# Optimization experiments

Hardware: AMD Instinct MI355X
Metric: run time of the kernel (lower is better)

The kernel has to match this reference:

```python
import jax, jax.numpy as jnp
import numpy as np

T, D, H, E, K = 8192, 2048, 7168, 8, 2


def setup_inputs() -> dict:
    key = jax.random.key(0)
    ks = jax.random.split(key, 5)
    s = 0.02
    return {
        "x": jax.random.normal(ks[0], (T, D), jnp.float32),
        "gate_w": jax.random.normal(ks[1], (E, D), jnp.float32) * s,
        "w1": jax.random.normal(ks[2], (E, H, D), jnp.float32) * s,
        "w2": jax.random.normal(ks[3], (E, H, D), jnp.float32) * s,
        "w3": jax.random.normal(ks[4], (E, H, D), jnp.float32) * s,
    }


def reference(x, gate_w, w1, w2, w3):
    # gate logits [T, E]
    logits = x @ gate_w.T
    vals, idx = jax.lax.top_k(logits, K)                      # [T, K]
    w = jax.nn.softmax(vals.astype(jnp.float32), axis=-1).astype(x.dtype)
    # per-token routing weight for each expert (0 if not selected) [T, E]
    tok = jnp.arange(x.shape[0])
    expert_w = jnp.zeros((x.shape[0], E), x.dtype).at[tok[:, None], idx].add(w)

    # scan over experts: dense SwiGLU per expert, weighted accumulate
    def body(acc, ws):
        w1e, w2e, w3e, we = ws  # [H,D],[H,D],[H,D],[T]
        y = (jax.nn.silu(x @ w1e.T) * (x @ w3e.T)) @ w2e      # [T, D]
        return acc + we[:, None] * y, None

    res, _ = jax.lax.scan(body, jnp.zeros_like(x), (w1, w2, w3, expert_w.T))
    return res
```

## Files before the change

kernel.cpp:

```cpp
#include <hip/hip_runtime.h>

#define TT   8192
#define DDIM 2048
#define HDIM 7168
#define NEXP 8
#define MT   32
#define NT1  (HDIM / 128)
#define NT2  (DDIM / 256)
#define NTILE_MAX 72

typedef __attribute__((ext_vector_type(8))) short bf16x8;
typedef __attribute__((ext_vector_type(8))) short short8v;
typedef __attribute__((ext_vector_type(4))) short short4v;
typedef __attribute__((ext_vector_type(4))) float f32x4;

__device__ __forceinline__ unsigned short f2bf(float f) {
  unsigned int u = __builtin_bit_cast(unsigned int, f);
  u += 0x7fffu + ((u >> 16) & 1u);
  return (unsigned short)(u >> 16);
}

__device__ __forceinline__ void gload_lds16(const void* gp, void* lp) {
  __builtin_amdgcn_global_load_lds((__attribute__((address_space(1))) void*)gp,
                                   (__attribute__((address_space(3))) void*)lp,
                                   16, 0, 0);
}

__device__ __forceinline__ void mfma16(f32x4& c, bf16x8 a, bf16x8 b) {
  c = __builtin_amdgcn_mfma_f32_16x16x32_bf16(a, b, c, 0, 0, 0);
}

__device__ __forceinline__ void wg_barrier() {
  asm volatile("" ::: "memory");
  __builtin_amdgcn_s_barrier();
  asm volatile("" ::: "memory");
}

#define PH(H, BA, BB, RDB, STG, SRCP, SOFF, VM)                              \
  do {                                                                       \
    if (RDB) {                                                               \
      _Pragma("unroll")                                                      \
      for (int n = 0; n < 4; ++n)                                            \
        bfr[n] = *(const bf16x8*)(smem + (BB) + rB + n * 1024);              \
    }                                                                        \
    _Pragma("unroll")                                                        \
    for (int m = 0; m < 4; ++m)                                              \
      af[m] = *(const bf16x8*)(smem + (BA) + rA + ((H) + m) * 1024);         \
    if ((STG) >= 0) {                                                        \
      gload_lds16(SRCP[0] + (SOFF), smem + (STG) + wid * 2048);              \
      gload_lds16(SRCP[1] + (SOFF), smem + (STG) + wid * 2048 + 1024);       \
    }                                                                        \
    wg_barrier();                                                            \
    __builtin_amdgcn_s_setprio(1);                                           \
    _Pragma("unroll")                                                        \
    for (int n = 0; n < 4; ++n) {                                            \
      _Pragma("unroll")                                                      \
      for (int m = 0; m < 4; ++m)                                            \
        mfma16(acc[(H) + m][n], af[m], bfr[n]);                              \
    }                                                                        \
    __builtin_amdgcn_s_setprio(0);                                           \
    if ((VM) == 6) asm volatile("s_waitcnt vmcnt(6)" ::: "memory");          \
    if ((VM) == 0) asm volatile("s_waitcnt vmcnt(0)" ::: "memory");          \
    wg_barrier();                                                            \
  } while (0)

#define ITER_FULL(kb)                                                        \
  PH(0, 0,     32768,  1, 81920,  asrc, (kb) + 192, -1);                     \
  PH(4, 0,     32768,  0, 32768,  bsrc, (kb) + 256, -1);                     \
  PH(0, 16384, 49152,  1, 0,      asrc, (kb) + 256, -1);                     \
  PH(4, 16384, 49152,  0, 49152,  bsrc, (kb) + 320,  6);                     \
  PH(0, 65536, 98304,  1, 16384,  asrc, (kb) + 320, -1);                     \
  PH(4, 65536, 98304,  0, 98304,  bsrc, (kb) + 384, -1);                     \
  PH(0, 81920, 114688, 1, 65536,  asrc, (kb) + 384, -1);                     \
  PH(4, 81920, 114688, 0, 114688, bsrc, (kb) + 448,  6);

#define ITER_LAST(kb)                                                        \
  PH(0, 0,     32768,  1, 81920,  asrc, (kb) + 192, -1);                     \
  PH(4, 0,     32768,  0, -1,     asrc, 0,          -1);                     \
  PH(0, 16384, 49152,  1, -1,     asrc, 0,          -1);                     \
  PH(4, 16384, 49152,  0, -1,     asrc, 0,           0);                     \
  PH(0, 65536, 98304,  1, -1,     asrc, 0,          -1);                     \
  PH(4, 65536, 98304,  0, -1,     asrc, 0,          -1);                     \
  PH(0, 81920, 114688, 1, -1,     asrc, 0,          -1);                     \
  PH(4, 81920, 114688, 0, -1,     asrc, 0,          -1);

#define PROLOGUE()                                                           \
  do {                                                                       \
    gload_lds16(asrc[0] + 0,   smem + 0      + wid * 2048);                  \
    gload_lds16(asrc[1] + 0,   smem + 0      + wid * 2048 + 1024);           \
    gload_lds16(bsrc[0] + 0,   smem + 32768  + wid * 2048);                  \
    gload_lds16(bsrc[1] + 0,   smem + 32768  + wid * 2048 + 1024);           \
    gload_lds16(asrc[0] + 64,  smem + 16384  + wid * 2048);                  \
    gload_lds16(asrc[1] + 64,  smem + 16384  + wid * 2048 + 1024);           \
    gload_lds16(bsrc[0] + 64,  smem + 49152  + wid * 2048);                  \
    gload_lds16(bsrc[1] + 64,  smem + 49152  + wid * 2048 + 1024);           \
    gload_lds16(bsrc[0] + 128, smem + 98304  + wid * 2048);                  \
    gload_lds16(bsrc[1] + 128, smem + 98304  + wid * 2048 + 1024);           \
    gload_lds16(asrc[0] + 128, smem + 65536  + wid * 2048);                  \
    gload_lds16(asrc[1] + 128, smem + 65536  + wid * 2048 + 1024);           \
    gload_lds16(bsrc[0] + 192, smem + 114688 + wid * 2048);                  \
    gload_lds16(bsrc[1] + 192, smem + 114688 + wid * 2048 + 1024);           \
    asm volatile("s_waitcnt vmcnt(6)" ::: "memory");                         \
    wg_barrier();                                                            \
  } while (0)

__global__ __launch_bounds__(256) void cvt_bf16_kernel(const float* __restrict__ src,
                                                       unsigned short* __restrict__ dst,
                                                       long n8) {
  long i = (long)blockIdx.x * 256 + threadIdx.x;
  long stride = (long)gridDim.x * 256;
  for (; i < n8; i += stride) {
    float4 a = ((const float4*)src)[i * 2];
    float4 b = ((const float4*)src)[i * 2 + 1];
    short8v s;
    s[0] = (short)f2bf(a.x); s[1] = (short)f2bf(a.y);
    s[2] = (short)f2bf(a.z); s[3] = (short)f2bf(a.w);
    s[4] = (short)f2bf(b.x); s[5] = (short)f2bf(b.y);
    s[6] = (short)f2bf(b.z); s[7] = (short)f2bf(b.w);
    ((short8v*)dst)[i] = s;
  }
}

__global__ __launch_bounds__(256) void gate_kernel(const float* __restrict__ x,
                                                   const float* __restrict__ gw,
                                                   int* __restrict__ route_e,
                                                   float* __restrict__ route_w,
                                                   int* __restrict__ counts) {
  int t = blockIdx.x;
  int tid = threadIdx.x;
  const float* xr = x + (size_t)t * DDIM;
  float p[NEXP];
#pragma unroll
  for (int e = 0; e < NEXP; ++e) p[e] = 0.f;
#pragma unroll
  for (int c = 0; c < DDIM / (256 * 4); ++c) {
    int d = (c * 256 + tid) * 4;
    float4 xv = *(const float4*)(xr + d);
#pragma unroll
    for (int e = 0; e < NEXP; ++e) {
      float4 wv = *(const float4*)(gw + (size_t)e * DDIM + d);
      p[e] += xv.x * wv.x + xv.y * wv.y + xv.z * wv.z + xv.w * wv.w;
    }
  }
  __shared__ float red[NEXP][4];
  int lane = tid & 63, wid = tid >> 6;
#pragma unroll
  for (int e = 0; e < NEXP; ++e) {
    float v = p[e];
    for (int o = 32; o > 0; o >>= 1) v += __shfl_down(v, o);
    if (lane == 0) red[e][wid] = v;
  }
  __syncthreads();
  if (tid == 0) {
    float lg[NEXP];
#pragma unroll
    for (int e = 0; e < NEXP; ++e) lg[e] = red[e][0] + red[e][1] + red[e][2] + red[e][3];
    int i0 = 0;
#pragma unroll
    for (int e = 1; e < NEXP; ++e) if (lg[e] > lg[i0]) i0 = e;
    int i1 = -1;
#pragma unroll
    for (int e = 0; e < NEXP; ++e) {
      if (e == i0) continue;
      if (i1 < 0 || lg[e] > lg[i1]) i1 = e;
    }
    float w0 = 1.f / (1.f + __expf(lg[i1] - lg[i0]));
    float w1 = 1.f - w0;
    route_e[t * 2 + 0] = i0;  route_e[t * 2 + 1] = i1;
    route_w[t * 2 + 0] = w0;  route_w[t * 2 + 1] = w1;
    atomicAdd(&counts[i0], 1);
    atomicAdd(&counts[i1], 1);
  }
}

__global__ void scan_kernel(const int* __restrict__ counts, int* __restrict__ offsets,
                            int* __restrict__ cursor, int* __restrict__ tmap) {
  if (threadIdx.x == 0 && blockIdx.x == 0) {
    int o = 0, idx = 0;
    for (int e = 0; e < NEXP; ++e) {
      offsets[e] = o; cursor[e] = o;
      int c = counts[e]; o += c;
      for (int t = 0; t * 256 < c && idx < NTILE_MAX; ++t) tmap[1 + idx++] = (e << 16) | t;
    }
    tmap[0] = idx;
  }
}

__global__ __launch_bounds__(256) void scatter_kernel(const int* __restrict__ route_e,
                                                      const float* __restrict__ route_w,
                                                      int* __restrict__ cursor,
                                                      int* __restrict__ tok_list,
                                                      float* __restrict__ tok_w) {
  int t = blockIdx.x * 256 + threadIdx.x;
  if (t >= TT) return;
#pragma unroll
  for (int s = 0; s < 2; ++s) {
    int e = route_e[t * 2 + s];
    int p = atomicAdd(&cursor[e], 1);
    tok_list[p] = t;
    tok_w[p] = route_w[t * 2 + s];
  }
}

__global__ __launch_bounds__(256) void transpose_w2_kernel(const float* __restrict__ w2,
                                                           unsigned short* __restrict__ w2t,
                                                           int expert_fixed) {
  int e = expert_fixed >= 0 ? expert_fixed : (int)blockIdx.z;
  const float* src = w2 + (size_t)e * HDIM * DDIM;
  unsigned short* dst = w2t + (expert_fixed >= 0 ? (size_t)0 : (size_t)e * DDIM * HDIM);
  int h0 = blockIdx.x * 64, d0 = blockIdx.y * 64;
  __shared__ __align__(8) unsigned short tile[64 * 66];
  int tid = threadIdx.x;
  int hr = tid >> 2;
#pragma unroll
  for (int j = 0; j < 4; ++j) {
    int f4 = (tid & 3) + j * 4;
    float4 v = *(const float4*)(src + (size_t)(h0 + hr) * DDIM + d0 + f4 * 4);
    unsigned int lo = (unsigned int)f2bf(v.x) | ((unsigned int)f2bf(v.y) << 16);
    unsigned int hi = (unsigned int)f2bf(v.z) | ((unsigned int)f2bf(v.w) << 16);
    char* bp = (char*)tile + hr * 132 + f4 * 8;
    *(unsigned int*)bp = lo;
    *(unsigned int*)(bp + 4) = hi;
  }
  __syncthreads();
  int dr = tid >> 2;
  int hbase = (tid & 3) * 16;
  unsigned short vals[16];
#pragma unroll
  for (int i = 0; i < 16; ++i)
    vals[i] = *(unsigned short*)((char*)tile + (hbase + i) * 132 + dr * 2);
  unsigned short* op = dst + (size_t)(d0 + dr) * HDIM + h0 + hbase;
  short8v s0, s1;
#pragma unroll
  for (int i = 0; i < 8; ++i) { s0[i] = (short)vals[i]; s1[i] = (short)vals[i + 8]; }
  *(short8v*)(op) = s0;
  *(short8v*)(op + 8) = s1;
}

__global__ __launch_bounds__(512, 2) void gemm1_kernel(
    const unsigned short* __restrict__ xbf, const unsigned short* __restrict__ w1b,
    const unsigned short* __restrict__ w3b, const int* __restrict__ tok_list,
    const int* __restrict__ counts, const int* __restrict__ offsets,
    const int* __restrict__ tmap,
    unsigned short* __restrict__ g, int expert_fixed) {
  __shared__ __align__(16) char smem[133120];
  constexpr int NI = DDIM / 128;

  int nwg = gridDim.x;
  int orig = blockIdx.x;
  int wg = (orig & 7) * (nwg >> 3) + (orig >> 3);
  int e, mbase, nt;
  if (expert_fixed >= 0) {
    e = expert_fixed;
    mbase = (wg & (MT - 1)) * 256;
    nt = (wg >> 5) % NT1;
  } else {
    int tl = wg % NTILE_MAX;
    nt = wg / NTILE_MAX;
    if (tl >= tmap[0]) return;
    int pk = tmap[1 + tl];
    e = pk >> 16;
    mbase = (pk & 0xffff) * 256;
  }
  int cnt = counts[e];
  if (mbase >= cnt) return;
  int off = offsets[e];
  int gshift = expert_fixed >= 0 ? 0 : off;
  int rows = cnt - mbase; if (rows > 256) rows = 256;

  const unsigned short* w1e = expert_fixed >= 0 ? w1b : w1b + (size_t)e * HDIM * DDIM;
  const unsigned short* w3e = expert_fixed >= 0 ? w3b : w3b + (size_t)e * HDIM * DDIM;

  int tid = threadIdx.x, lane = tid & 63, wid = tid >> 6;
  int wr = wid >> 2, wc = wid & 3;

  int r16 = lane >> 2;
  int csrc = (lane & 3) ^ ((lane >> 3) & 3);
  const char* asrc[2]; const char* bsrc[2];
#pragma unroll
  for (int j = 0; j < 2; ++j) {
    int r = wid * 32 + j * 16 + r16;
    int m = mbase + r; if (m > cnt - 1) m = cnt - 1;
    int tok = tok_list[off + m];
    asrc[j] = (const char*)xbf + (size_t)tok * (DDIM * 2) + csrc * 16;
    const char* base = (r < 128)
        ? (const char*)w1e + (size_t)(nt * 128 + r) * (DDIM * 2)
        : (const char*)w3e + (size_t)(nt * 128 + r - 128) * (DDIM * 2);
    bsrc[j] = base + csrc * 16;
  }
  int rA = (wr * 128 + (lane & 15)) * 64 + (((lane >> 4) ^ ((lane >> 1) & 3)) * 16);
  int rB = (wc * 64  + (lane & 15)) * 64 + (((lane >> 4) ^ ((lane >> 1) & 3)) * 16);

  f32x4 zv = {0.f, 0.f, 0.f, 0.f};
  f32x4 acc[8][4];
#pragma unroll
  for (int m = 0; m < 8; ++m)
#pragma unroll
    for (int n = 0; n < 4; ++n) acc[m][n] = zv;
  bf16x8 af[4], bfr[4];

  PROLOGUE();
#pragma unroll 1
  for (int i = 0; i < NI - 1; ++i) {
    size_t kb = (size_t)i * 256;
    ITER_FULL(kb);
  }
  {
    size_t kb = (size_t)(NI - 1) * 256;
    ITER_LAST(kb);
  }

  float* hb = (float*)smem;
  if (wc < 2) {
#pragma unroll
    for (int m = 0; m < 8; ++m)
#pragma unroll
      for (int q = 0; q < 4; ++q) {
        int row = wr * 128 + m * 16 + (lane >> 4) * 4 + q;
        int col = wc * 64 + (lane & 15);
#pragma unroll
        for (int n = 0; n < 4; ++n)
          hb[row * 130 + col + n * 16] = acc[m][n][q];
      }
  }
  asm volatile("s_waitcnt lgkmcnt(0)" ::: "memory");
  wg_barrier();
  if (wc >= 2) {
#pragma unroll
    for (int m = 0; m < 8; ++m)
#pragma unroll
      for (int q = 0; q < 4; ++q) {
        int row = wr * 128 + m * 16 + (lane >> 4) * 4 + q;
        if (row >= rows) continue;
        size_t grow = (size_t)(mbase + row + gshift);
        int colbase = (wc - 2) * 64 + (lane & 15);
        unsigned short* gp = g + grow * HDIM + nt * 128 + colbase;
#pragma unroll
        for (int n = 0; n < 4; ++n) {
          float h1 = hb[row * 130 + colbase + n * 16];
          float h3 = acc[m][n][q];
          float gv = (h1 / (1.f + __expf(-h1))) * h3;
          gp[n * 16] = f2bf(gv);
        }
      }
  }
}

__global__ __launch_bounds__(512, 2) void gemm2_kernel(
    const unsigned short* __restrict__ g, const unsigned short* __restrict__ w2t,
    const int* __restrict__ tok_list, const float* __restrict__ tok_w,
    const int* __restrict__ counts, const int* __restrict__ offsets,
    const int* __restrict__ tmap,
    float* __restrict__ out, int expert_fixed) {
  __shared__ __align__(16) char smem[131072];
  constexpr int NI = HDIM / 128;

  int nwg = gridDim.x;
  int orig = blockIdx.x;
  int wg = (orig & 7) * (nwg >> 3) + (orig >> 3);
  int e, mbase, nt;
  if (expert_fixed >= 0) {
    e = expert_fixed;
    mbase = (wg & (MT - 1)) * 256;
    nt = (wg >> 5) % NT2;
  } else {
    int tl = wg % NTILE_MAX;
    nt = wg / NTILE_MAX;
    if (tl >= tmap[0]) return;
    int pk = tmap[1 + tl];
    e = pk >> 16;
    mbase = (pk & 0xffff) * 256;
  }
  int cnt = counts[e];
  if (mbase >= cnt) return;
  int off = offsets[e];
  int gshift = expert_fixed >= 0 ? 0 : off;
  int nbase = nt * 256;
  int rows = cnt - mbase; if (rows > 256) rows = 256;
  const unsigned short* w2te = w2t + (expert_fixed >= 0 ? (size_t)0 : (size_t)e * DDIM * HDIM);

  int tid = threadIdx.x, lane = tid & 63, wid = tid >> 6;
  int wr = wid >> 2, wc = wid & 3;

  int r16 = lane >> 2;
  int csrc = (lane & 3) ^ ((lane >> 3) & 3);
  const char* asrc[2]; const char* bsrc[2];
#pragma unroll
  for (int j = 0; j < 2; ++j) {
    int r = wid * 32 + j * 16 + r16;
    int m = mbase + r; if (m > cnt - 1) m = cnt - 1;
    asrc[j] = (const char*)g + (size_t)(m + gshift) * (HDIM * 2) + csrc * 16;
    bsrc[j] = (const char*)w2te + (size_t)(nbase + r) * (HDIM * 2) + csrc * 16;
  }
  int rA = (wr * 128 + (lane & 15)) * 64 + (((lane >> 4) ^ ((lane >> 1) & 3)) * 16);
  int rB = (wc * 64  + (lane & 15)) * 64 + (((lane >> 4) ^ ((lane >> 1) & 3)) * 16);

  f32x4 zv = {0.f, 0.f, 0.f, 0.f};
  f32x4 acc[8][4];
#pragma unroll
  for (int m = 0; m < 8; ++m)
#pragma unroll
    for (int n = 0; n < 4; ++n) acc[m][n] = zv;
  bf16x8 af[4], bfr[4];

  PROLOGUE();
#pragma unroll 1
  for (int i = 0; i < NI - 1; ++i) {
    size_t kb = (size_t)i * 256;
    ITER_FULL(kb);
  }
  {
    size_t kb = (size_t)(NI - 1) * 256;
    ITER_LAST(kb);
  }

#pragma unroll
  for (int m = 0; m < 8; ++m)
#pragma unroll
    for (int q = 0; q < 4; ++q) {
      int row = wr * 128 + m * 16 + (lane >> 4) * 4 + q;
      if (row >= rows) continue;
      int mi = mbase + row;
      int tok = tok_list[off + mi];
      float wt = tok_w[off + mi];
      float* op = out + (size_t)tok * DDIM + nbase + wc * 64 + (lane & 15);
#pragma unroll
      for (int n = 0; n < 4; ++n)
        atomicAdd(op + n * 16, acc[m][n][q] * wt);
    }
}

extern "C" void kernel_launch(void* const* d_in, const int* in_sizes, int n_in,
                              void* d_out, int out_size, void* d_ws, size_t ws_size,
                              hipStream_t stream) {
  const float* x      = (const float*)d_in[0];
  const float* gate_w = (const float*)d_in[1];
  const float* w1     = (const float*)d_in[2];
  const float* w2     = (const float*)d_in[3];
  const float* w3     = (const float*)d_in[4];
  float* out = (float*)d_out;
  char* ws = (char*)d_ws;

  size_t o = 0;
  int* counts  = (int*)(ws + o);
  int* offsets = counts + 8;
  int* cursor  = counts + 16;
  int* tmap    = counts + 24;
  o += 1024;
  int*   route_e = (int*)(ws + o);   o += (size_t)TT * 2 * 4;
  float* route_w = (float*)(ws + o); o += (size_t)TT * 2 * 4;
  int*   tok_list = (int*)(ws + o);  o += (size_t)TT * 2 * 4;
  float* tok_w = (float*)(ws + o);   o += (size_t)TT * 2 * 4;
  unsigned short* xbf = (unsigned short*)(ws + o); o += (size_t)TT * DDIM * 2;
  size_t fixed = o;

  const size_t WSZ = (size_t)HDIM * DDIM;
  const size_t wbf_full = (size_t)NEXP * WSZ * 2;
  const size_t gfull = (size_t)TT * 2 * HDIM * 2;

  hipMemsetAsync(counts, 0, 8 * sizeof(int), stream);
  hipMemsetAsync(out, 0, (size_t)TT * DDIM * sizeof(float), stream);
  cvt_bf16_kernel<<<4096, 256, 0, stream>>>(x, xbf, (long)TT * DDIM / 8);
  gate_kernel<<<TT, 256, 0, stream>>>(x, gate_w, route_e, route_w, counts);
  scan_kernel<<<1, 64, 0, stream>>>(counts, offsets, cursor, tmap);
  scatter_kernel<<<(TT + 255) / 256, 256, 0, stream>>>(route_e, route_w, cursor, tok_list, tok_w);

  if (ws_size >= fixed + 3 * wbf_full + gfull) {
    unsigned short* w1b = (unsigned short*)(ws + fixed);
    unsigned short* w3b = w1b + NEXP * WSZ;
    unsigned short* w2t = w3b + NEXP * WSZ;
    unsigned short* gbuf = w2t + NEXP * WSZ;
    cvt_bf16_kernel<<<8192, 256, 0, stream>>>(w1, w1b, (long)(NEXP * WSZ / 8));
    cvt_bf16_kernel<<<8192, 256, 0, stream>>>(w3, w3b, (long)(NEXP * WSZ / 8));
    transpose_w2_kernel<<<dim3(HDIM / 64, DDIM / 64, NEXP), 256, 0, stream>>>(w2, w2t, -1);
    gemm1_kernel<<<NTILE_MAX * NT1, 512, 0, stream>>>(
        xbf, w1b, w3b, tok_list, counts, offsets, tmap, gbuf, -1);
    gemm2_kernel<<<NTILE_MAX * NT2, 512, 0, stream>>>(
        gbuf, w2t, tok_list, tok_w, counts, offsets, tmap, out, -1);
  } else {
    unsigned short* w1b = (unsigned short*)(ws + fixed);
    unsigned short* w3b = w1b + WSZ;
    unsigned short* w2t = w3b + WSZ;
    unsigned short* gbuf = w2t + WSZ;
    for (int e = 0; e < NEXP; ++e) {
      cvt_bf16_kernel<<<4096, 256, 0, stream>>>(w1 + (size_t)e * WSZ, w1b, (long)(WSZ / 8));
      cvt_bf16_kernel<<<4096, 256, 0, stream>>>(w3 + (size_t)e * WSZ, w3b, (long)(WSZ / 8));
      transpose_w2_kernel<<<dim3(HDIM / 64, DDIM / 64, 1), 256, 0, stream>>>(w2, w2t, e);
      gemm1_kernel<<<MT * NT1, 512, 0, stream>>>(
          xbf, w1b, w3b, tok_list, counts, offsets, tmap, gbuf, e);
      gemm2_kernel<<<MT * NT2, 512, 0, stream>>>(
          gbuf, w2t, tok_list, tok_w, counts, offsets, tmap, out, e);
    }
  }
}
```

Baseline: 2.297 ms.

## Replace gemm2 atomic scatter-add with bf16 slot buffer plus per-token reduce

The second GEMM now writes each routed row's output as bf16 into a per-slot buffer (reusing the w1 bf16 region) instead of doing fp32 atomicAdds into the output. A new reduce kernel combines each token's two slots using the routing weights, which also removes the full output memset on the main path. The gemm2 tile index mapping is also reordered so consecutive workgroups share the same row tile across N tiles. The cost is an extra kernel and bf16 rounding of the per-expert outputs before they are combined.

```diff
diff --git a/kernel.cpp b/kernel.cpp
--- a/kernel.cpp
+++ b/kernel.cpp
@@ -18,6 +18,11 @@
   unsigned int u = __builtin_bit_cast(unsigned int, f);
   u += 0x7fffu + ((u >> 16) & 1u);
   return (unsigned short)(u >> 16);
+}
+
+__device__ __forceinline__ float bf2f(unsigned short h) {
+  unsigned int u = ((unsigned int)h) << 16;
+  return __builtin_bit_cast(float, u);
 }
 
 __device__ __forceinline__ void gload_lds16(const void* gp, void* lp) {
@@ -190,7 +195,8 @@
                                                       const float* __restrict__ route_w,
                                                       int* __restrict__ cursor,
                                                       int* __restrict__ tok_list,
-                                                      float* __restrict__ tok_w) {
+                                                      float* __restrict__ tok_w,
+                                                      int* __restrict__ slot_of) {
   int t = blockIdx.x * 256 + threadIdx.x;
   if (t >= TT) return;
 #pragma unroll
@@ -199,6 +205,7 @@
     int p = atomicAdd(&cursor[e], 1);
     tok_list[p] = t;
     tok_w[p] = route_w[t * 2 + s];
+    slot_of[t * 2 + s] = p;
   }
 }
 
@@ -235,6 +242,30 @@
   for (int i = 0; i < 8; ++i) { s0[i] = (short)vals[i]; s1[i] = (short)vals[i + 8]; }
   *(short8v*)(op) = s0;
   *(short8v*)(op + 8) = s1;
+}
+
+__global__ __launch_bounds__(256) void reduce_kernel(const unsigned short* __restrict__ ybuf,
+                                                     const int* __restrict__ slot_of,
+                                                     const float* __restrict__ route_w,
+                                                     float* __restrict__ out) {
+  int t = blockIdx.x;
+  int d = threadIdx.x * 8;
+  int s0 = slot_of[t * 2 + 0], s1 = slot_of[t * 2 + 1];
+  float w0 = route_w[t * 2 + 0], w1 = route_w[t * 2 + 1];
+  bf16x8 y0 = *(const bf16x8*)(ybuf + (size_t)s0 * DDIM + d);
+  bf16x8 y1 = *(const bf16x8*)(ybuf + (size_t)s1 * DDIM + d);
+  float4 o0, o1;
+  o0.x = w0 * bf2f((unsigned short)y0[0]) + w1 * bf2f((unsigned short)y1[0]);
+  o0.y = w0 * bf2f((unsigned short)y0[1]) + w1 * bf2f((unsigned short)y1[1]);
+  o0.z = w0 * bf2f((unsigned short)y0[2]) + w1 * bf2f((unsigned short)y1[2]);
+  o0.w = w0 * bf2f((unsigned short)y0[3]) + w1 * bf2f((unsigned short)y1[3]);
+  o1.x = w0 * bf2f((unsigned short)y0[4]) + w1 * bf2f((unsigned short)y1[4]);
+  o1.y = w0 * bf2f((unsigned short)y0[5]) + w1 * bf2f((unsigned short)y1[5]);
+  o1.z = w0 * bf2f((unsigned short)y0[6]) + w1 * bf2f((unsigned short)y1[6]);
+  o1.w = w0 * bf2f((unsigned short)y0[7]) + w1 * bf2f((unsigned short)y1[7]);
+  float* op = out + (size_t)t * DDIM + d;
+  *(float4*)op = o0;
+  *(float4*)(op + 4) = o1;
 }
 
 __global__ __launch_bounds__(512, 2) void gemm1_kernel(
@@ -351,7 +382,7 @@
     const int* __restrict__ tok_list, const float* __restrict__ tok_w,
     const int* __restrict__ counts, const int* __restrict__ offsets,
     const int* __restrict__ tmap,
-    float* __restrict__ out, int expert_fixed) {
+    unsigned short* __restrict__ ybuf, float* __restrict__ out, int expert_fixed) {
   __shared__ __align__(16) char smem[131072];
   constexpr int NI = HDIM / 128;
 
@@ -361,11 +392,11 @@
   int e, mbase, nt;
   if (expert_fixed >= 0) {
     e = expert_fixed;
-    mbase = (wg & (MT - 1)) * 256;
-    nt = (wg >> 5) % NT2;
+    nt = wg % NT2;
+    mbase = (wg / NT2) * 256;
   } else {
-    int tl = wg % NTILE_MAX;
-    nt = wg / NTILE_MAX;
+    int tl = wg / NT2;
+    nt = wg % NT2;
     if (tl >= tmap[0]) return;
     int pk = tmap[1 + tl];
     e = pk >> 16;
@@ -414,20 +445,35 @@
     ITER_LAST(kb);
   }
 
-#pragma unroll
-  for (int m = 0; m < 8; ++m)
-#pragma unroll
-    for (int q = 0; q < 4; ++q) {
-      int row = wr * 128 + m * 16 + (lane >> 4) * 4 + q;
-      if (row >= rows) continue;
-      int mi = mbase + row;
-      int tok = tok_list[off + mi];
-      float wt = tok_w[off + mi];
-      float* op = out + (size_t)tok * DDIM + nbase + wc * 64 + (lane & 15);
-#pragma unroll
-      for (int n = 0; n < 4; ++n)
-        atomicAdd(op + n * 16, acc[m][n][q] * wt);
-    }
+  if (ybuf) {
+#pragma unroll
+    for (int m = 0; m < 8; ++m)
+#pragma unroll
+      for (int q = 0; q < 4; ++q) {
+        int row = wr * 128 + m * 16 + (lane >> 4) * 4 + q;
+        if (row >= rows) continue;
+        size_t slot = (size_t)(off + mbase + row);
+        unsigned short* yp = ybuf + slot * DDIM + nbase + wc * 64 + (lane & 15);
+#pragma unroll
+        for (int n = 0; n < 4; ++n)
+          yp[n * 16] = f2bf(acc[m][n][q]);
+      }
+  } else {
+#pragma unroll
+    for (int m = 0; m < 8; ++m)
+#pragma unroll
+      for (int q = 0; q < 4; ++q) {
+        int row = wr * 128 + m * 16 + (lane >> 4) * 4 + q;
+        if (row >= rows) continue;
+        int mi = mbase + row;
+        int tok = tok_list[off + mi];
+        float wt = tok_w[off + mi];
+        float* op = out + (size_t)tok * DDIM + nbase + wc * 64 + (lane & 15);
+#pragma unroll
+        for (int n = 0; n < 4; ++n)
+          atomicAdd(op + n * 16, acc[m][n][q] * wt);
+      }
+  }
 }
 
 extern "C" void kernel_launch(void* const* d_in, const int* in_sizes, int n_in,
@@ -451,6 +497,7 @@
   float* route_w = (float*)(ws + o); o += (size_t)TT * 2 * 4;
   int*   tok_list = (int*)(ws + o);  o += (size_t)TT * 2 * 4;
   float* tok_w = (float*)(ws + o);   o += (size_t)TT * 2 * 4;
+  int*   slot_of = (int*)(ws + o);   o += (size_t)TT * 2 * 4;
   unsigned short* xbf = (unsigned short*)(ws + o); o += (size_t)TT * DDIM * 2;
   size_t fixed = o;
 
@@ -459,29 +506,32 @@
   const size_t gfull = (size_t)TT * 2 * HDIM * 2;
 
   hipMemsetAsync(counts, 0, 8 * sizeof(int), stream);
-  hipMemsetAsync(out, 0, (size_t)TT * DDIM * sizeof(float), stream);
   cvt_bf16_kernel<<<4096, 256, 0, stream>>>(x, xbf, (long)TT * DDIM / 8);
   gate_kernel<<<TT, 256, 0, stream>>>(x, gate_w, route_e, route_w, counts);
   scan_kernel<<<1, 64, 0, stream>>>(counts, offsets, cursor, tmap);
-  scatter_kernel<<<(TT + 255) / 256, 256, 0, stream>>>(route_e, route_w, cursor, tok_list, tok_w);
+  scatter_kernel<<<(TT + 255) / 256, 256, 0, stream>>>(route_e, route_w, cursor,
+                                                       tok_list, tok_w, slot_of);
 
   if (ws_size >= fixed + 3 * wbf_full + gfull) {
     unsigned short* w1b = (unsigned short*)(ws + fixed);
     unsigned short* w3b = w1b + NEXP * WSZ;
     unsigned short* w2t = w3b + NEXP * WSZ;
     unsigned short* gbuf = w2t + NEXP * WSZ;
+    unsigned short* ybuf = w1b;
     cvt_bf16_kernel<<<8192, 256, 0, stream>>>(w1, w1b, (long)(NEXP * WSZ / 8));
     cvt_bf16_kernel<<<8192, 256, 0, stream>>>(w3, w3b, (long)(NEXP * WSZ / 8));
     transpose_w2_kernel<<<dim3(HDIM / 64, DDIM / 64, NEXP), 256, 0, stream>>>(w2, w2t, -1);
     gemm1_kernel<<<NTILE_MAX * NT1, 512, 0, stream>>>(
         xbf, w1b, w3b, tok_list, counts, offsets, tmap, gbuf, -1);
     gemm2_kernel<<<NTILE_MAX * NT2, 512, 0, stream>>>(
-        gbuf, w2t, tok_list, tok_w, counts, offsets, tmap, out, -1);
+        gbuf, w2t, tok_list, tok_w, counts, offsets, tmap, ybuf, out, -1);
+    reduce_kernel<<<TT, 256, 0, stream>>>(ybuf, slot_of, route_w, out);
   } else {
     unsigned short* w1b = (unsigned short*)(ws + fixed);
     unsigned short* w3b = w1b + WSZ;
     unsigned short* w2t = w3b + WSZ;
     unsigned short* gbuf = w2t + WSZ;
+    hipMemsetAsync(out, 0, (size_t)TT * DDIM * sizeof(float), stream);
     for (int e = 0; e < NEXP; ++e) {
       cvt_bf16_kernel<<<4096, 256, 0, stream>>>(w1 + (size_t)e * WSZ, w1b, (long)(WSZ / 8));
       cvt_bf16_kernel<<<4096, 256, 0, stream>>>(w3 + (size_t)e * WSZ, w3b, (long)(WSZ / 8));
@@ -489,7 +539,7 @@
       gemm1_kernel<<<MT * NT1, 512, 0, stream>>>(
           xbf, w1b, w3b, tok_list, counts, offsets, tmap, gbuf, e);
       gemm2_kernel<<<MT * NT2, 512, 0, stream>>>(
-          gbuf, w2t, tok_list, tok_w, counts, offsets, tmap, out, e);
+          gbuf, w2t, tok_list, tok_w, counts, offsets, tmap, (unsigned short*)0, out, e);
     }
   }
 }
```

After: 2.254 ms. Within noise of the previous version (-1.9%).
